# Performance work log

Measured on AMD Instinct MI355X. Metric: run time of the kernel, lower is better.

Reference implementation:

```python
import jax, jax.numpy as jnp
import numpy as np

D = 1024
H = 16
DH = D // H  # 64
EPS = 1e-5


def _ln(x, w, b=None):
    mu = jnp.mean(x, axis=-1, keepdims=True)
    var = jnp.var(x, axis=-1, keepdims=True)
    y = (x - mu) * jax.lax.rsqrt(var + EPS) * w
    return y + b if b is not None else y


def _rotate_half(x):
    x1, x2 = jnp.split(x, 2, axis=-1)
    return jnp.concatenate([-x2, x1], axis=-1)


def _rope(q, k):
    # q, k: [B, L, H, DH]; rotary over sequence dim (ESM-style half-split rotation)
    L = q.shape[1]
    inv_freq = 1.0 / (10000.0 ** (jnp.arange(0, DH, 2, dtype=jnp.float32) / DH))
    freqs = jnp.arange(L, dtype=jnp.float32)[:, None] * inv_freq[None, :]  # [L, DH/2]
    emb = jnp.concatenate([freqs, freqs], axis=-1)  # [L, DH]
    cos = jnp.cos(emb)[None, :, None, :]  # [1, L, 1, DH]
    sin = jnp.sin(emb)[None, :, None, :]
    q = q * cos + _rotate_half(q) * sin
    k = k * cos + _rotate_half(k) * sin
    return q, k


def setup_inputs() -> dict:
    key = jax.random.key(0)
    ks = jax.random.split(key, 8)
    B, L = 2, 2048
    x = jax.random.normal(ks[0], (B, L, D), dtype=jnp.float32)
    seq_id = jnp.sort(jax.random.randint(ks[1], (B, L), 0, 8), axis=-1)
    s = 1.0 / np.sqrt(D)
    return {
        "x": x,
        "seq_id": seq_id,
        "ln1_w": jnp.ones((D,), jnp.float32),
        "ln1_b": jnp.zeros((D,), jnp.float32),
        "w_qkv": jax.random.normal(ks[2], (3 * D, D), dtype=jnp.float32) * s,
        "q_ln_w": jnp.ones((D,), jnp.float32),
        "k_ln_w": jnp.ones((D,), jnp.float32),
        "out_w": jax.random.normal(ks[3], (D, D), dtype=jnp.float32) * s,
    }


def reference(x, seq_id, ln1_w, ln1_b, w_qkv, q_ln_w, k_ln_w, out_w):
    B, L, _ = x.shape
    h = _ln(x, ln1_w, ln1_b)
    qkv = jnp.einsum("bld,ed->ble", h, w_qkv)  # [B, L, 3D]
    q, k, v = jnp.split(qkv, 3, axis=-1)
    q = _ln(q, q_ln_w)
    k = _ln(k, k_ln_w)
    q = q.reshape(B, L, H, DH)
    k = k.reshape(B, L, H, DH)
    q, k = _rope(q, k)
    q = q.transpose(0, 2, 1, 3)  # [B, H, L, DH]
    k = k.transpose(0, 2, 1, 3)
    v = v.reshape(B, L, H, DH).transpose(0, 2, 1, 3)
    scale = 1.0 / np.sqrt(DH)
    scores = jnp.einsum("bhld,bhmd->bhlm", q, k) * scale  # [B, H, L, L]
    mask = (seq_id[:, None, :, None] == seq_id[:, None, None, :])  # [B, 1, L, L]
    scores = jnp.where(mask, scores, -jnp.inf)
    attn = jax.nn.softmax(scores, axis=-1)
    ctx = jnp.einsum("bhlm,bhmd->bhld", attn, v)  # [B, H, L, DH]
    ctx = ctx.transpose(0, 2, 1, 3).reshape(B, L, D)
    return jnp.einsum("bld,ed->ble", ctx, out_w)
```

## Files before the change

kernel.cpp:

```cpp
#include <hip/hip_runtime.h>
#include <hip/hip_bf16.h>
#include <math.h>

#define D 1024
#define H 16
#define DH 64
#define L 2048
#define B 2
#define NROW (B * L)
#define EPS 1e-5f

typedef _Float16 half8 __attribute__((ext_vector_type(8)));
typedef _Float16 half4v __attribute__((ext_vector_type(4)));
typedef float f32x4 __attribute__((ext_vector_type(4)));

__global__ __launch_bounds__(256) void prep_kernel(const float* __restrict__ x,
                                                   const float* __restrict__ lw,
                                                   const float* __restrict__ lb,
                                                   _Float16* __restrict__ h16,
                                                   const float* __restrict__ wqkv,
                                                   _Float16* __restrict__ wqkv16,
                                                   const float* __restrict__ outw,
                                                   _Float16* __restrict__ outw16,
                                                   const int* __restrict__ seq_id,
                                                   int* __restrict__ lo,
                                                   int* __restrict__ hi,
                                                   float2* __restrict__ rtab) {
    int blk = blockIdx.x;
    int t = threadIdx.x;
    if (blk < 4096) {
        int r = blk;
        const float* xr = x + (size_t)r * D;
        float4 v = *(const float4*)&xr[t * 4];
        float s = v.x + v.y + v.z + v.w;
        float sq = v.x * v.x + v.y * v.y + v.z * v.z + v.w * v.w;
        for (int off = 32; off > 0; off >>= 1) {
            s += __shfl_xor(s, off, 64);
            sq += __shfl_xor(sq, off, 64);
        }
        __shared__ float ls[4], lq[4];
        int wave = t >> 6;
        if ((t & 63) == 0) { ls[wave] = s; lq[wave] = sq; }
        __syncthreads();
        float S = ls[0] + ls[1] + ls[2] + ls[3];
        float Q = lq[0] + lq[1] + lq[2] + lq[3];
        float mu = S / (float)D;
        float rs = rsqrtf(Q / (float)D - mu * mu + EPS);
        float4 w4 = *(const float4*)&lw[t * 4];
        float4 b4 = *(const float4*)&lb[t * 4];
        half4v o = {(_Float16)((v.x - mu) * rs * w4.x + b4.x),
                    (_Float16)((v.y - mu) * rs * w4.y + b4.y),
                    (_Float16)((v.z - mu) * rs * w4.z + b4.z),
                    (_Float16)((v.w - mu) * rs * w4.w + b4.w)};
        *(half4v*)&h16[(size_t)r * D + t * 4] = o;
    } else if (blk < 6144) {
        int base = blk - 4096;
        const float* src;
        _Float16* dst;
        if (base < 1536) { src = wqkv; dst = wqkv16; }
        else             { src = outw; dst = outw16; base -= 1536; }
        int i = (base * 256 + t) * 8;
        float4 a = *(const float4*)&src[i];
        float4 b = *(const float4*)&src[i + 4];
        half8 h = {(_Float16)a.x, (_Float16)a.y, (_Float16)a.z, (_Float16)a.w,
                   (_Float16)b.x, (_Float16)b.y, (_Float16)b.z, (_Float16)b.w};
        *(half8*)&dst[i] = h;
    } else if (blk < 6160) {
        int idx = (blk - 6144) * 256 + t;
        int b = idx / L, l = idx - b * L;
        const int* row = seq_id + (size_t)b * L;
        int v = row[l];
        int a = 0, c = L;
        while (a < c) { int m = (a + c) >> 1; if (row[m] < v) a = m + 1; else c = m; }
        lo[idx] = a;
        a = 0; c = L;
        while (a < c) { int m = (a + c) >> 1; if (row[m] <= v) a = m + 1; else c = m; }
        hi[idx] = a;
    } else {
        int idx = (blk - 6160) * 256 + t;
        int l = idx >> 5, fi = idx & 31;
        float invf = expf(-(float)fi * 0.28782313662425572f);
        float sn, cs;
        sincosf((float)l * invf, &sn, &cs);
        rtab[idx] = make_float2(cs, sn);
    }
}

template <typename OutT, int BM, int BN>
__global__ __launch_bounds__(256) void gemm_f16_kernel(const _Float16* __restrict__ A,
                                                       const _Float16* __restrict__ W,
                                                       OutT* __restrict__ C, int N) {
    constexpr int WM = BM / 2, WN = BN / 2;
    constexpr int MT = WM / 16, NT = WN / 16;
    __shared__ _Float16 As[2][BM * 32];
    __shared__ _Float16 Bs[2][BN * 32];
    int t = threadIdx.x;
    int w = t >> 6, lane = t & 63;
    int quad = lane >> 4, col = lane & 15;
    int m0 = blockIdx.y * BM, n0 = blockIdx.x * BN;
    int mw = (w >> 1) * WM, nw = (w & 1) * WN;
    int sw = (col >> 1) & 3;

    f32x4 acc[MT][NT] = {};

    auto stage = [&](int k0, int buf) {
#pragma unroll
        for (int i = 0; i < BM / 64; i++) {
            int e = t + i * 256;
            int row = e >> 2, kc = (e & 3) ^ ((row >> 1) & 3);
            __builtin_amdgcn_global_load_lds(
                (const __attribute__((address_space(1))) void*)&A[(size_t)(m0 + row) * 1024 + k0 + kc * 8],
                (__attribute__((address_space(3))) void*)&As[buf][e * 8], 16, 0, 0);
        }
#pragma unroll
        for (int i = 0; i < BN / 64; i++) {
            int e = t + i * 256;
            int row = e >> 2, kc = (e & 3) ^ ((row >> 1) & 3);
            __builtin_amdgcn_global_load_lds(
                (const __attribute__((address_space(1))) void*)&W[(size_t)(n0 + row) * 1024 + k0 + kc * 8],
                (__attribute__((address_space(3))) void*)&Bs[buf][e * 8], 16, 0, 0);
        }
    };

    stage(0, 0);
    int cur = 0;
    for (int k0 = 0; k0 < 1024; k0 += 32) {
        __syncthreads();
        if (k0 + 32 < 1024) stage(k0 + 32, cur ^ 1);
        half8 af[MT], bf[NT];
#pragma unroll
        for (int mt = 0; mt < MT; mt++)
            af[mt] = *(const half8*)&As[cur][(mw + mt * 16 + col) * 32 + ((quad ^ sw) << 3)];
#pragma unroll
        for (int nt = 0; nt < NT; nt++)
            bf[nt] = *(const half8*)&Bs[cur][(nw + nt * 16 + col) * 32 + ((quad ^ sw) << 3)];
#pragma unroll
        for (int mt = 0; mt < MT; mt++)
#pragma unroll
            for (int nt = 0; nt < NT; nt++)
                acc[mt][nt] = __builtin_amdgcn_mfma_f32_16x16x32_f16(af[mt], bf[nt], acc[mt][nt], 0, 0, 0);
        cur ^= 1;
    }

#pragma unroll
    for (int mt = 0; mt < MT; mt++)
#pragma unroll
        for (int nt = 0; nt < NT; nt++)
#pragma unroll
            for (int r = 0; r < 4; r++) {
                int row = m0 + mw + mt * 16 + quad * 4 + r;
                int cc = n0 + nw + nt * 16 + col;
                C[(size_t)row * N + cc] = (OutT)acc[mt][nt][r];
            }
}

__global__ __launch_bounds__(256) void mid_kernel(const _Float16* __restrict__ qkv,
                                                  const float* __restrict__ qw,
                                                  const float* __restrict__ kw,
                                                  const float2* __restrict__ rtab,
                                                  _Float16* __restrict__ q_r,
                                                  _Float16* __restrict__ k_r,
                                                  _Float16* __restrict__ v_t) {
    __shared__ float ls[4], lq[4];
    __shared__ _Float16 T[64][72];
    int blk = blockIdx.x;
    int t = threadIdx.x;
    if (blk < 8192) {
        int r = blk >> 1;
        int which = blk & 1;
        const _Float16* src = qkv + (size_t)r * 3072 + which * 1024;
        const float* w = which ? kw : qw;
        _Float16* dst = which ? k_r : q_r;

        float vals[4];
        float s = 0.f, sq = 0.f;
#pragma unroll
        for (int i = 0; i < 4; i++) {
            float v = (float)src[t + i * 256];
            vals[i] = v;
            s += v;
            sq += v * v;
        }
        for (int off = 32; off > 0; off >>= 1) {
            s += __shfl_xor(s, off, 64);
            sq += __shfl_xor(sq, off, 64);
        }
        int wave = t >> 6;
        if ((t & 63) == 0) { ls[wave] = s; lq[wave] = sq; }
        __syncthreads();
        float S = ls[0] + ls[1] + ls[2] + ls[3];
        float Q = lq[0] + lq[1] + lq[2] + lq[3];
        float mu = S / 1024.f;
        float rs = rsqrtf(Q / 1024.f - mu * mu + EPS);

        int l = r & (L - 1);
        int b = r >> 11;
#pragma unroll
        for (int i = 0; i < 4; i++) {
            int j = t + i * 256;
            float y = (vals[i] - mu) * rs * w[j];
            float p = __shfl_xor(y, 32, 64);
            int dh = j & 63, hh = j >> 6;
            float2 cs = rtab[l * 32 + (dh & 31)];
            float out = (dh < 32) ? (y * cs.x - p * cs.y) : (y * cs.x + p * cs.y);
            dst[((size_t)((b * H + hh) * L + l)) * 64 + dh] = (_Float16)out;
        }
    } else {
        int vb = blk - 8192;
        int bh = vb >> 5;
        int b = bh >> 4, h = bh & 15;
        int l0 = (vb & 31) * 64;
#pragma unroll
        for (int i = 0; i < 2; i++) {
            int e = t + i * 256;
            int li = e >> 3, ch = e & 7;
            half8 hv = *(const half8*)&qkv[((size_t)(b * L + l0 + li)) * 3072 + 2048 + h * 64 + ch * 8];
            *(half8*)&T[li][ch * 8] = hv;
        }
        __syncthreads();
#pragma unroll
        for (int i = 0; i < 2; i++) {
            int e = t + i * 256;
            int d = e >> 3, ch = e & 7;
            half8 hv;
#pragma unroll
            for (int j = 0; j < 8; j++) hv[j] = T[ch * 8 + j][d];
            *(half8*)&v_t[((size_t)(bh * 64 + d)) * 2048 + l0 + ch * 8] = hv;
        }
    }
}

__global__ __launch_bounds__(256) void attn_mfma_kernel(const _Float16* __restrict__ q_r,
                                                        const _Float16* __restrict__ k_r,
                                                        const _Float16* __restrict__ v_t,
                                                        const int* __restrict__ lo_arr,
                                                        const int* __restrict__ hi_arr,
                                                        _Float16* __restrict__ ctx) {
    __shared__ _Float16 Ks[64][72];
    __shared__ _Float16 VsT[64][72];
    __shared__ _Float16 Ps[4][16][72];
    int bh = blockIdx.y;
    int b = bh >> 4, h = bh & 15;
    int l0 = blockIdx.x * 64;
    int t = threadIdx.x;
    int w = t >> 6, lane = t & 63;
    int quad = lane >> 4, col = lane & 15;
    int rbase = l0 + w * 16;

    half8 qf0, qf1;
    {
        const _Float16* qp = q_r + ((size_t)(bh * L + rbase + col)) * 64 + quad * 8;
        qf0 = *(const half8*)qp;
        qf1 = *(const half8*)(qp + 32);
    }
    int myrow = rbase + quad * 4;
    int lo_r[4], hi_r[4];
#pragma unroll
    for (int r = 0; r < 4; r++) {
        lo_r[r] = lo_arr[b * L + myrow + r];
        hi_r[r] = hi_arr[b * L + myrow + r];
    }

    f32x4 o[4] = {{0.f, 0.f, 0.f, 0.f}, {0.f, 0.f, 0.f, 0.f},
                  {0.f, 0.f, 0.f, 0.f}, {0.f, 0.f, 0.f, 0.f}};
    float m_run[4], l_run[4];
#pragma unroll
    for (int r = 0; r < 4; r++) { m_run[r] = -1e30f; l_run[r] = 0.f; }

    int blo = lo_arr[b * L + l0] & ~63;
    int bhi = hi_arr[b * L + l0 + 63];
    const float SCL = 0.125f * 1.4426950408889634f;

    for (int m0 = blo; m0 < bhi; m0 += 64) {
#pragma unroll
        for (int i = 0; i < 2; i++) {
            int e = t + i * 256;
            int row = e >> 3, ch = e & 7;
            *(uint4*)&Ks[row][ch * 8] =
                *(const uint4*)&k_r[((size_t)(bh * L + m0 + row)) * 64 + ch * 8];
            *(uint4*)&VsT[row][ch * 8] =
                *(const uint4*)&v_t[((size_t)(bh * 64 + row)) * 2048 + m0 + ch * 8];
        }
        __syncthreads();

        f32x4 s[4] = {{0.f, 0.f, 0.f, 0.f}, {0.f, 0.f, 0.f, 0.f},
                      {0.f, 0.f, 0.f, 0.f}, {0.f, 0.f, 0.f, 0.f}};
#pragma unroll
        for (int nt = 0; nt < 4; nt++) {
            const _Float16* kp = &Ks[nt * 16 + col][quad * 8];
            half8 kf0 = *(const half8*)kp;
            half8 kf1 = *(const half8*)(kp + 32);
            s[nt] = __builtin_amdgcn_mfma_f32_16x16x32_f16(qf0, kf0, s[nt], 0, 0, 0);
            s[nt] = __builtin_amdgcn_mfma_f32_16x16x32_f16(qf1, kf1, s[nt], 0, 0, 0);
        }

        float p[4][4];
#pragma unroll
        for (int nt = 0; nt < 4; nt++) {
            int key = m0 + nt * 16 + col;
#pragma unroll
            for (int r = 0; r < 4; r++) {
                float v = s[nt][r] * SCL;
                p[nt][r] = (key >= lo_r[r] && key < hi_r[r]) ? v : -INFINITY;
            }
        }

        float corr[4];
#pragma unroll
        for (int r = 0; r < 4; r++) {
            float rm = fmaxf(fmaxf(p[0][r], p[1][r]), fmaxf(p[2][r], p[3][r]));
#pragma unroll
            for (int off = 1; off < 16; off <<= 1) rm = fmaxf(rm, __shfl_xor(rm, off, 64));
            float nm = fmaxf(m_run[r], rm);
            corr[r] = exp2f(m_run[r] - nm);
            m_run[r] = nm;
            float rs = 0.f;
#pragma unroll
            for (int nt = 0; nt < 4; nt++) {
                float e = exp2f(p[nt][r] - nm);
                p[nt][r] = e;
                rs += e;
            }
#pragma unroll
            for (int off = 1; off < 16; off <<= 1) rs += __shfl_xor(rs, off, 64);
            l_run[r] = l_run[r] * corr[r] + rs;
        }

#pragma unroll
        for (int nt = 0; nt < 4; nt++)
#pragma unroll
            for (int r = 0; r < 4; r++) {
                o[nt][r] *= corr[r];
                Ps[w][quad * 4 + r][nt * 16 + col] = (_Float16)p[nt][r];
            }

        half8 pf0 = *(const half8*)&Ps[w][col][quad * 8];
        half8 pf1 = *(const half8*)&Ps[w][col][32 + quad * 8];
#pragma unroll
        for (int nt = 0; nt < 4; nt++) {
            const _Float16* vp = &VsT[nt * 16 + col][quad * 8];
            half8 vf0 = *(const half8*)vp;
            half8 vf1 = *(const half8*)(vp + 32);
            o[nt] = __builtin_amdgcn_mfma_f32_16x16x32_f16(pf0, vf0, o[nt], 0, 0, 0);
            o[nt] = __builtin_amdgcn_mfma_f32_16x16x32_f16(pf1, vf1, o[nt], 0, 0, 0);
        }
        __syncthreads();
    }

#pragma unroll
    for (int nt = 0; nt < 4; nt++)
#pragma unroll
        for (int r = 0; r < 4; r++) {
            int row = myrow + r;
            ctx[((size_t)(b * L + row)) * 1024 + h * 64 + nt * 16 + col] =
                (_Float16)(o[nt][r] / l_run[r]);
        }
}

extern "C" void kernel_launch(void* const* d_in, const int* in_sizes, int n_in,
                              void* d_out, int out_size, void* d_ws, size_t ws_size,
                              hipStream_t stream) {
    const float* x      = (const float*)d_in[0];
    const int*   seq_id = (const int*)d_in[1];
    const float* ln1_w  = (const float*)d_in[2];
    const float* ln1_b  = (const float*)d_in[3];
    const float* w_qkv  = (const float*)d_in[4];
    const float* q_ln_w = (const float*)d_in[5];
    const float* k_ln_w = (const float*)d_in[6];
    const float* out_w  = (const float*)d_in[7];
    float* out = (float*)d_out;

    char* ws = (char*)d_ws;
    int*      lo     = (int*)(ws);
    int*      hi     = (int*)(ws + (64 << 10));
    float2*   rtab   = (float2*)(ws + (128 << 10));
    _Float16* h16    = (_Float16*)(ws + (1ull << 20));
    _Float16* wqkv16 = (_Float16*)(ws + (10ull << 20));
    _Float16* outw16 = (_Float16*)(ws + (17ull << 20));
    _Float16* qkv16  = (_Float16*)(ws + (20ull << 20));
    _Float16* q_r    = (_Float16*)(ws + (45ull << 20));
    _Float16* k_r    = (_Float16*)(ws + (54ull << 20));
    _Float16* v_t    = (_Float16*)(ws + (63ull << 20));
    _Float16* ctx16  = (_Float16*)(ws + (72ull << 20));

    prep_kernel<<<dim3(6416), dim3(256), 0, stream>>>(
        x, ln1_w, ln1_b, h16, w_qkv, wqkv16, out_w, outw16, seq_id, lo, hi, rtab);
    gemm_f16_kernel<_Float16, 128, 128><<<dim3(3072 / 128, NROW / 128), dim3(256), 0, stream>>>(
        h16, wqkv16, qkv16, 3072);
    mid_kernel<<<dim3(9216), dim3(256), 0, stream>>>(qkv16, q_ln_w, k_ln_w, rtab, q_r, k_r, v_t);
    attn_mfma_kernel<<<dim3(L / 64, B * H), dim3(256), 0, stream>>>(q_r, k_r, v_t, lo, hi, ctx16);
    gemm_f16_kernel<float, 128, 64><<<dim3(1024 / 64, NROW / 128), dim3(256), 0, stream>>>(
        ctx16, outw16, out, 1024);

    (void)in_sizes; (void)n_in; (void)out_size; (void)ws_size;
}
```

Measured before the change: 197.5 us.

## Double-buffer attention K/V tiles with async LDS loads and XOR swizzle

The attention kernel now stages K/V tiles directly into shared memory via global_load_lds into two buffers, prefetching the next tile while the current one is computed. Padding is replaced by an XOR swizzle in the K, V, P and transpose buffers. The QK MFMA operands are swapped so each lane owns one query row, which simplifies the softmax reductions to two shuffles, and masking is skipped for tiles fully inside the segment. This targets load latency, LDS bank conflicts and shuffle overhead, at the cost of more index arithmetic and reliance on matching swizzles between the load and read sides.

```diff
diff --git a/kernel.cpp b/kernel.cpp
--- a/kernel.cpp
+++ b/kernel.cpp
@@ -162,7 +162,7 @@
                                                   _Float16* __restrict__ k_r,
                                                   _Float16* __restrict__ v_t) {
     __shared__ float ls[4], lq[4];
-    __shared__ _Float16 T[64][72];
+    __shared__ _Float16 T[64][64];
     int blk = blockIdx.x;
     int t = threadIdx.x;
     if (blk < 8192) {
@@ -215,7 +215,7 @@
             int e = t + i * 256;
             int li = e >> 3, ch = e & 7;
             half8 hv = *(const half8*)&qkv[((size_t)(b * L + l0 + li)) * 3072 + 2048 + h * 64 + ch * 8];
-            *(half8*)&T[li][ch * 8] = hv;
+            *(half8*)&T[li][((ch ^ (li >> 3)) & 7) * 8] = hv;
         }
         __syncthreads();
 #pragma unroll
@@ -224,7 +224,8 @@
             int d = e >> 3, ch = e & 7;
             half8 hv;
 #pragma unroll
-            for (int j = 0; j < 8; j++) hv[j] = T[ch * 8 + j][d];
+            for (int j = 0; j < 8; j++)
+                hv[j] = T[ch * 8 + j][((((d >> 3) ^ ch) & 7) * 8) + (d & 7)];
             *(half8*)&v_t[((size_t)(bh * 64 + d)) * 2048 + l0 + ch * 8] = hv;
         }
     }
@@ -236,9 +237,9 @@
                                                         const int* __restrict__ lo_arr,
                                                         const int* __restrict__ hi_arr,
                                                         _Float16* __restrict__ ctx) {
-    __shared__ _Float16 Ks[64][72];
-    __shared__ _Float16 VsT[64][72];
-    __shared__ _Float16 Ps[4][16][72];
+    __shared__ _Float16 Ks[2][64][64];
+    __shared__ _Float16 Vs[2][64][64];
+    __shared__ _Float16 Ps[4][16][64];
     int bh = blockIdx.y;
     int b = bh >> 4, h = bh & 15;
     int l0 = blockIdx.x * 64;
@@ -247,114 +248,137 @@
     int quad = lane >> 4, col = lane & 15;
     int rbase = l0 + w * 16;
 
+    int blo = lo_arr[b * L + l0] & ~63;
+    int bhi = hi_arr[b * L + l0 + 63];
+
+    auto stage = [&](int m0, int buf) {
+#pragma unroll
+        for (int i = 0; i < 2; i++) {
+            int e = t + i * 256;
+            int row = e >> 3, ch = e & 7;
+            int sch = ch ^ (row & 7);
+            __builtin_amdgcn_global_load_lds(
+                (const __attribute__((address_space(1))) void*)&k_r[((size_t)(bh * L + m0 + row)) * 64 + sch * 8],
+                (__attribute__((address_space(3))) void*)&Ks[buf][row][ch * 8], 16, 0, 0);
+            __builtin_amdgcn_global_load_lds(
+                (const __attribute__((address_space(1))) void*)&v_t[((size_t)(bh * 64 + row)) * 2048 + m0 + sch * 8],
+                (__attribute__((address_space(3))) void*)&Vs[buf][row][ch * 8], 16, 0, 0);
+        }
+    };
+
+    stage(blo, 0);
+
     half8 qf0, qf1;
     {
         const _Float16* qp = q_r + ((size_t)(bh * L + rbase + col)) * 64 + quad * 8;
         qf0 = *(const half8*)qp;
         qf1 = *(const half8*)(qp + 32);
     }
-    int myrow = rbase + quad * 4;
-    int lo_r[4], hi_r[4];
-#pragma unroll
-    for (int r = 0; r < 4; r++) {
-        lo_r[r] = lo_arr[b * L + myrow + r];
-        hi_r[r] = hi_arr[b * L + myrow + r];
-    }
-
-    f32x4 o[4] = {{0.f, 0.f, 0.f, 0.f}, {0.f, 0.f, 0.f, 0.f},
-                  {0.f, 0.f, 0.f, 0.f}, {0.f, 0.f, 0.f, 0.f}};
-    float m_run[4], l_run[4];
-#pragma unroll
-    for (int r = 0; r < 4; r++) { m_run[r] = -1e30f; l_run[r] = 0.f; }
-
-    int blo = lo_arr[b * L + l0] & ~63;
-    int bhi = hi_arr[b * L + l0 + 63];
+    int lo_c = lo_arr[b * L + rbase + col];
+    int hi_c = hi_arr[b * L + rbase + col];
+    int wlo = __shfl(lo_c, 15, 64);
+    int whi = __shfl(hi_c, 0, 64);
+
+    f32x4 o[4] = {};
+    float m_run = -1e30f, l_run = 0.f;
     const float SCL = 0.125f * 1.4426950408889634f;
-
+    int swz = (col & 7) << 3;
+    int src = (lane & 48) | ((lane & 48) >> 2);
+
+    int cur = 0;
     for (int m0 = blo; m0 < bhi; m0 += 64) {
-#pragma unroll
-        for (int i = 0; i < 2; i++) {
-            int e = t + i * 256;
-            int row = e >> 3, ch = e & 7;
-            *(uint4*)&Ks[row][ch * 8] =
-                *(const uint4*)&k_r[((size_t)(bh * L + m0 + row)) * 64 + ch * 8];
-            *(uint4*)&VsT[row][ch * 8] =
-                *(const uint4*)&v_t[((size_t)(bh * 64 + row)) * 2048 + m0 + ch * 8];
-        }
         __syncthreads();
-
-        f32x4 s[4] = {{0.f, 0.f, 0.f, 0.f}, {0.f, 0.f, 0.f, 0.f},
-                      {0.f, 0.f, 0.f, 0.f}, {0.f, 0.f, 0.f, 0.f}};
+        if (m0 + 64 < bhi) stage(m0 + 64, cur ^ 1);
+
+        f32x4 s[4] = {};
 #pragma unroll
         for (int nt = 0; nt < 4; nt++) {
-            const _Float16* kp = &Ks[nt * 16 + col][quad * 8];
-            half8 kf0 = *(const half8*)kp;
-            half8 kf1 = *(const half8*)(kp + 32);
-            s[nt] = __builtin_amdgcn_mfma_f32_16x16x32_f16(qf0, kf0, s[nt], 0, 0, 0);
-            s[nt] = __builtin_amdgcn_mfma_f32_16x16x32_f16(qf1, kf1, s[nt], 0, 0, 0);
+            int key = nt * 16 + col;
+            const _Float16* kp = &Ks[cur][key][0];
+            half8 kf0 = *(const half8*)&kp[(quad ^ (key & 7)) * 8];
+            half8 kf1 = *(const half8*)&kp[((quad + 4) ^ (key & 7)) * 8];
+            s[nt] = __builtin_amdgcn_mfma_f32_16x16x32_f16(kf0, qf0, s[nt], 0, 0, 0);
+            s[nt] = __builtin_amdgcn_mfma_f32_16x16x32_f16(kf1, qf1, s[nt], 0, 0, 0);
         }
 
         float p[4][4];
+        bool full = (m0 >= wlo) && (m0 + 64 <= whi);
+        if (full) {
+#pragma unroll
+            for (int nt = 0; nt < 4; nt++)
+#pragma unroll
+                for (int r = 0; r < 4; r++) p[nt][r] = s[nt][r] * SCL;
+        } else {
+#pragma unroll
+            for (int nt = 0; nt < 4; nt++) {
+                int kb = m0 + nt * 16 + quad * 4;
+#pragma unroll
+                for (int r = 0; r < 4; r++) {
+                    int key = kb + r;
+                    p[nt][r] = (key >= lo_c && key < hi_c) ? s[nt][r] * SCL : -INFINITY;
+                }
+            }
+        }
+
+        float tmax = p[0][0];
+#pragma unroll
+        for (int nt = 0; nt < 4; nt++)
+#pragma unroll
+            for (int r = 0; r < 4; r++) tmax = fmaxf(tmax, p[nt][r]);
+        tmax = fmaxf(tmax, __shfl_xor(tmax, 16, 64));
+        tmax = fmaxf(tmax, __shfl_xor(tmax, 32, 64));
+        float nm = fmaxf(m_run, tmax);
+        float corr = exp2f(m_run - nm);
+        m_run = nm;
+        float rs = 0.f;
+#pragma unroll
+        for (int nt = 0; nt < 4; nt++)
+#pragma unroll
+            for (int r = 0; r < 4; r++) {
+                float e2 = exp2f(p[nt][r] - nm);
+                p[nt][r] = e2;
+                rs += e2;
+            }
+        rs += __shfl_xor(rs, 16, 64);
+        rs += __shfl_xor(rs, 32, 64);
+        l_run = l_run * corr + rs;
+
 #pragma unroll
         for (int nt = 0; nt < 4; nt++) {
-            int key = m0 + nt * 16 + col;
-#pragma unroll
-            for (int r = 0; r < 4; r++) {
-                float v = s[nt][r] * SCL;
-                p[nt][r] = (key >= lo_r[r] && key < hi_r[r]) ? v : -INFINITY;
-            }
-        }
-
-        float corr[4];
+            half4v pk = {(_Float16)p[nt][0], (_Float16)p[nt][1],
+                         (_Float16)p[nt][2], (_Float16)p[nt][3]};
+            *(half4v*)&Ps[w][col][(nt * 16 + quad * 4) ^ swz] = pk;
+        }
+
 #pragma unroll
         for (int r = 0; r < 4; r++) {
-            float rm = fmaxf(fmaxf(p[0][r], p[1][r]), fmaxf(p[2][r], p[3][r]));
-#pragma unroll
-            for (int off = 1; off < 16; off <<= 1) rm = fmaxf(rm, __shfl_xor(rm, off, 64));
-            float nm = fmaxf(m_run[r], rm);
-            corr[r] = exp2f(m_run[r] - nm);
-            m_run[r] = nm;
-            float rs = 0.f;
-#pragma unroll
-            for (int nt = 0; nt < 4; nt++) {
-                float e = exp2f(p[nt][r] - nm);
-                p[nt][r] = e;
-                rs += e;
-            }
-#pragma unroll
-            for (int off = 1; off < 16; off <<= 1) rs += __shfl_xor(rs, off, 64);
-            l_run[r] = l_run[r] * corr[r] + rs;
-        }
-
-#pragma unroll
-        for (int nt = 0; nt < 4; nt++)
-#pragma unroll
-            for (int r = 0; r < 4; r++) {
-                o[nt][r] *= corr[r];
-                Ps[w][quad * 4 + r][nt * 16 + col] = (_Float16)p[nt][r];
-            }
-
-        half8 pf0 = *(const half8*)&Ps[w][col][quad * 8];
-        half8 pf1 = *(const half8*)&Ps[w][col][32 + quad * 8];
+            float c4 = __shfl(corr, src + r, 64);
+            o[0][r] *= c4; o[1][r] *= c4; o[2][r] *= c4; o[3][r] *= c4;
+        }
+
+        half8 pf0 = *(const half8*)&Ps[w][col][(quad * 8) ^ swz];
+        half8 pf1 = *(const half8*)&Ps[w][col][(32 + quad * 8) ^ swz];
 #pragma unroll
         for (int nt = 0; nt < 4; nt++) {
-            const _Float16* vp = &VsT[nt * 16 + col][quad * 8];
-            half8 vf0 = *(const half8*)vp;
-            half8 vf1 = *(const half8*)(vp + 32);
+            int dr = nt * 16 + col;
+            const _Float16* vp = &Vs[cur][dr][0];
+            half8 vf0 = *(const half8*)&vp[(quad ^ (dr & 7)) * 8];
+            half8 vf1 = *(const half8*)&vp[((quad + 4) ^ (dr & 7)) * 8];
             o[nt] = __builtin_amdgcn_mfma_f32_16x16x32_f16(pf0, vf0, o[nt], 0, 0, 0);
             o[nt] = __builtin_amdgcn_mfma_f32_16x16x32_f16(pf1, vf1, o[nt], 0, 0, 0);
         }
-        __syncthreads();
-    }
-
-#pragma unroll
-    for (int nt = 0; nt < 4; nt++)
-#pragma unroll
-        for (int r = 0; r < 4; r++) {
-            int row = myrow + r;
+        cur ^= 1;
+    }
+
+#pragma unroll
+    for (int r = 0; r < 4; r++) {
+        float linv = 1.f / __shfl(l_run, src + r, 64);
+        int row = rbase + quad * 4 + r;
+#pragma unroll
+        for (int nt = 0; nt < 4; nt++)
             ctx[((size_t)(b * L + row)) * 1024 + h * 64 + nt * 16 + col] =
-                (_Float16)(o[nt][r] / l_run[r]);
-        }
+                (_Float16)(o[nt][r] * linv);
+    }
 }
 
 extern "C" void kernel_launch(void* const* d_in, const int* in_sizes, int n_in,
```

After: 190.2 us. -3.7%, faster.
